# Optimization experiments

Measured on AMD Instinct MI355X. Metric: run time of the kernel, lower is better.

## Reference

```python
import jax, jax.numpy as jnp
import numpy as np

B, T, D = 8, 2048, 1024
E = 8               # num_experts
H = D // 8          # bottleneck dim = round(n_embed / reduction_rate) = 128


def setup_inputs() -> dict:
    key = jax.random.key(0)
    ks = jax.random.split(key, 7)
    s = 0.02
    return {
        "x":  jax.random.normal(ks[0], (B, T, D), dtype=jnp.float32),
        "Wr": jax.random.normal(ks[1], (D, E), dtype=jnp.float32) * s,
        "br": jnp.zeros((E,), dtype=jnp.float32),
        "Wd": jax.random.normal(ks[2], (E, D, H), dtype=jnp.float32) * s,
        "bd": jax.random.normal(ks[3], (E, H), dtype=jnp.float32) * s,
        "Wu": jax.random.normal(ks[4], (E, H, D), dtype=jnp.float32) * s,
        "bu": jax.random.normal(ks[5], (E, D), dtype=jnp.float32) * s,
    }


def reference(x, Wr, br, Wd, bd, Wu, bu):
    # Router: softmax over experts  -> [B, T, E]
    probs = jax.nn.softmax(x @ Wr + br, axis=-1)
    # All experts densely: down -> GELU (exact, matching torch.nn.GELU) -> up
    down = jnp.einsum('btd,edh->bteh', x, Wd) + bd            # [B, T, E, H]
    up = jnp.einsum('bteh,ehd->bted', jax.nn.gelu(down, approximate=False), Wu) + bu  # [B, T, E, D]
    # Router-weighted sum over experts -> [B, T, D]
    out = jnp.einsum('bte,bted->btd', probs, up)
    return out
```

## Files before the change

### kernel.cpp

```cpp
#include <hip/hip_runtime.h>

#define DEV __device__ __forceinline__

typedef short bf16x8 __attribute__((ext_vector_type(8)));
typedef float f32x4  __attribute__((ext_vector_type(4)));
typedef unsigned short u16;
typedef unsigned int u32;

constexpr int MTOK = 16384;
constexpr int DDIM = 1024;
constexpr int HDIM = 128;

constexpr int BM = 256, BN = 128, BK = 64;
constexpr int NKT = DDIM / BK;
constexpr int TA = BM * BK * 2;
constexpr int TB = BN * BK * 2;
constexpr int TT = TA + TB;

DEV u16 f2bf(float f) {
  u32 u = __builtin_bit_cast(u32, f);
  return (u16)((u + 0x7FFFu + ((u >> 16) & 1u)) >> 16);
}

DEV void async16(const void* g, void* l) {
  __builtin_amdgcn_global_load_lds(
      (const __attribute__((address_space(1))) void*)g,
      (__attribute__((address_space(3))) void*)l, 16, 0, 0);
}

__global__ __launch_bounds__(256) void prep_all_kernel(
    const float* __restrict__ x, const float* __restrict__ Wr,
    const float* __restrict__ br, const float* __restrict__ Wd,
    const float* __restrict__ Wu,
    u16* __restrict__ xh, u16* __restrict__ bdh, u16* __restrict__ wuh,
    float* __restrict__ probs)
{
  __shared__ float tl[32][33];
  const int bid = blockIdx.x;

  if (bid < 4096) {
    const int wave = threadIdx.x >> 6, lane = threadIdx.x & 63;
    const int t = bid * 4 + wave;
    const float* xr = x + (size_t)t * DDIM;

    float racc[8];
#pragma unroll
    for (int e = 0; e < 8; ++e) racc[e] = 0.f;

#pragma unroll
    for (int i = 0; i < 4; ++i) {
      const int d0 = i * 256 + lane * 4;
      float4 v = *(const float4*)(xr + d0);
      float vv[4] = {v.x, v.y, v.z, v.w};
      u16 hb[4];
#pragma unroll
      for (int j = 0; j < 4; ++j) {
        hb[j] = f2bf(vv[j]);
        const float4* w4 = (const float4*)(Wr + (size_t)(d0 + j) * 8);
        float4 w0 = w4[0], w1 = w4[1];
        racc[0] += vv[j] * w0.x; racc[1] += vv[j] * w0.y;
        racc[2] += vv[j] * w0.z; racc[3] += vv[j] * w0.w;
        racc[4] += vv[j] * w1.x; racc[5] += vv[j] * w1.y;
        racc[6] += vv[j] * w1.z; racc[7] += vv[j] * w1.w;
      }
      *(ushort4*)(xh + (size_t)t * DDIM + d0) = make_ushort4(hb[0], hb[1], hb[2], hb[3]);
    }

#pragma unroll
    for (int off = 32; off; off >>= 1)
#pragma unroll
      for (int e = 0; e < 8; ++e) racc[e] += __shfl_xor(racc[e], off, 64);

    float lg[8], mx = -1e30f;
#pragma unroll
    for (int e = 0; e < 8; ++e) { lg[e] = racc[e] + br[e]; mx = fmaxf(mx, lg[e]); }
    float ex[8], s = 0.f;
#pragma unroll
    for (int e = 0; e < 8; ++e) { ex[e] = expf(lg[e] - mx); s += ex[e]; }
    if (lane < 8) probs[(size_t)t * 8 + lane] = ex[lane] / s;
    return;
  }

  const float* src; u16* dst; int C; size_t dbase; int c0, r0;
  if (bid < 5120) {
    const int l = bid - 4096, e = l >> 7;
    src = Wd + (size_t)e * DDIM * HDIM; C = HDIM;
    dst = bdh; dbase = (size_t)e * HDIM * 1024;
    c0 = (l & 3) * 32; r0 = ((l >> 2) & 31) * 32;
  } else {
    const int l = bid - 5120, e = l >> 7;
    src = Wu + (size_t)e * HDIM * DDIM; C = DDIM;
    dst = wuh; dbase = (size_t)e * HDIM;
    c0 = (l & 31) * 32; r0 = ((l >> 5) & 3) * 32;
  }
  const int tx = threadIdx.x & 31, ty = threadIdx.x >> 5;
#pragma unroll
  for (int i = 0; i < 4; ++i)
    tl[ty + i * 8][tx] = src[(size_t)(r0 + ty + i * 8) * C + c0 + tx];
  __syncthreads();
#pragma unroll
  for (int i = 0; i < 4; ++i) {
    float v = tl[tx][ty + i * 8];
    dst[dbase + (size_t)(c0 + ty + i * 8) * 1024 + r0 + tx] = f2bf(v);
  }
}

template <int EPI>
__global__ __launch_bounds__(512, 2) void gemm_bf16_kernel(
    const u16* __restrict__ A, const u16* __restrict__ B,
    const float* __restrict__ bias, const float* __restrict__ probs,
    u16* __restrict__ ogp, float* __restrict__ of)
{
  __shared__ __align__(128) u16 lds[3 * TT / 2];
  const int tid = threadIdx.x, lane = tid & 63, wave = tid >> 6;
  const int wm = wave >> 1, wn = wave & 1;
  const int fr = lane & 15, fq = lane >> 4;

  const int swz = (blockIdx.x & 7) * 64 + (blockIdx.x >> 3);
  const int n0 = (swz >> 6) * BN;
  const int m0 = (swz & 63) * BM;

  auto stage = [&](int t) {
    u16* buf = lds + (size_t)(t % 3) * (TT / 2);
    const int kt = t * BK;
#pragma unroll
    for (int r = 0; r < 4; ++r) {
      const int off = r * 8192 + tid * 16;
      const int row = off >> 7, c = (off >> 4) & 7;
      const int sc = c ^ (row & 7);
      async16(A + (size_t)(m0 + row) * DDIM + kt + sc * 8, (char*)buf + off);
    }
#pragma unroll
    for (int r = 0; r < 2; ++r) {
      const int off = r * 8192 + tid * 16;
      const int row = off >> 7, c = (off >> 4) & 7;
      const int sc = c ^ (row & 7);
      async16(B + (size_t)(n0 + row) * DDIM + kt + sc * 8, (char*)buf + TA + off);
    }
  };

  f32x4 acc[4][4] = {};

  stage(0);
  stage(1);
  asm volatile("s_waitcnt vmcnt(6)" ::: "memory");
  __builtin_amdgcn_s_barrier();
  __builtin_amdgcn_sched_barrier(0);

  for (int t = 0; t < NKT; ++t) {
    if (t + 2 < NKT) stage(t + 2);

    const u16* At = lds + (size_t)(t % 3) * (TT / 2);
    const u16* Bt = At + TA / 2;
    bf16x8 a[2][4], b[2][4];
#pragma unroll
    for (int k2 = 0; k2 < 2; ++k2) {
      const int koff = k2 * 32 + fq * 8;
#pragma unroll
      for (int mi = 0; mi < 4; ++mi) {
        const int row = wm * 64 + mi * 16 + fr;
        int byt = (row << 7) + (koff << 1); byt ^= (row & 7) << 4;
        a[k2][mi] = *(const bf16x8*)((const char*)At + byt);
      }
#pragma unroll
      for (int ni = 0; ni < 4; ++ni) {
        const int row = wn * 64 + ni * 16 + fr;
        int byt = (row << 7) + (koff << 1); byt ^= (row & 7) << 4;
        b[k2][ni] = *(const bf16x8*)((const char*)Bt + byt);
      }
    }
    __builtin_amdgcn_s_setprio(1);
#pragma unroll
    for (int k2 = 0; k2 < 2; ++k2)
#pragma unroll
      for (int mi = 0; mi < 4; ++mi)
#pragma unroll
        for (int ni = 0; ni < 4; ++ni)
          acc[mi][ni] = __builtin_amdgcn_mfma_f32_16x16x32_bf16(
              a[k2][mi], b[k2][ni], acc[mi][ni], 0, 0, 0);
    __builtin_amdgcn_s_setprio(0);
    __builtin_amdgcn_sched_barrier(0);
    if (t < NKT - 2) asm volatile("s_waitcnt vmcnt(6)" ::: "memory");
    else             asm volatile("s_waitcnt vmcnt(0)" ::: "memory");
    __builtin_amdgcn_s_barrier();
    __builtin_amdgcn_sched_barrier(0);
  }

  if (EPI == 0) {
#pragma unroll
    for (int mi = 0; mi < 4; ++mi)
#pragma unroll
      for (int ni = 0; ni < 4; ++ni) {
        const int col = n0 + wn * 64 + ni * 16 + fr;
        const float bv = bias[col];
        const int e = col >> 7;
#pragma unroll
        for (int j = 0; j < 4; ++j) {
          const int row = m0 + wm * 64 + mi * 16 + fq * 4 + j;
          float v = acc[mi][ni][j] + bv;
          float g = 0.5f * v * (1.0f + erff(v * 0.70710678118654752f));
          ogp[(size_t)row * DDIM + col] = f2bf(probs[(size_t)row * 8 + e] * g);
        }
      }
  } else {
    float buv[4][8];
#pragma unroll
    for (int ni = 0; ni < 4; ++ni) {
      const int col = n0 + wn * 64 + ni * 16 + fr;
#pragma unroll
      for (int e = 0; e < 8; ++e) buv[ni][e] = bias[e * 1024 + col];
    }
#pragma unroll
    for (int mi = 0; mi < 4; ++mi)
#pragma unroll
      for (int j = 0; j < 4; ++j) {
        const int row = m0 + wm * 64 + mi * 16 + fq * 4 + j;
        const float4* pp = (const float4*)(probs + (size_t)row * 8);
        float4 p0 = pp[0], p1 = pp[1];
        float pr[8] = {p0.x, p0.y, p0.z, p0.w, p1.x, p1.y, p1.z, p1.w};
#pragma unroll
        for (int ni = 0; ni < 4; ++ni) {
          float v = acc[mi][ni][j];
#pragma unroll
          for (int e = 0; e < 8; ++e) v += pr[e] * buv[ni][e];
          of[(size_t)row * DDIM + n0 + wn * 64 + ni * 16 + fr] = v;
        }
      }
  }
}

extern "C" void kernel_launch(void* const* d_in, const int* in_sizes, int n_in,
                              void* d_out, int out_size, void* d_ws, size_t ws_size,
                              hipStream_t stream)
{
  const float* x  = (const float*)d_in[0];
  const float* Wr = (const float*)d_in[1];
  const float* br = (const float*)d_in[2];
  const float* Wd = (const float*)d_in[3];
  const float* bd = (const float*)d_in[4];
  const float* Wu = (const float*)d_in[5];
  const float* bu = (const float*)d_in[6];
  float* out = (float*)d_out;

  char* ws = (char*)d_ws;
  size_t off = 0;
  auto alloc = [&](size_t bytes) -> void* {
    void* p = ws + off;
    off += (bytes + 255) & ~(size_t)255;
    return p;
  };
  u16* xh  = (u16*)alloc((size_t)MTOK * DDIM * 2);
  u16* gph = (u16*)alloc((size_t)MTOK * 1024 * 2);
  u16* bdh = (u16*)alloc((size_t)1024 * 1024 * 2);
  u16* wuh = (u16*)alloc((size_t)1024 * 1024 * 2);
  float* probs = (float*)alloc((size_t)MTOK * 8 * 4);
  (void)ws_size; (void)in_sizes; (void)n_in; (void)out_size;

  prep_all_kernel<<<6144, 256, 0, stream>>>(x, Wr, br, Wd, Wu, xh, bdh, wuh, probs);

  gemm_bf16_kernel<0><<<512, 512, 0, stream>>>(xh, bdh, bd, probs, gph, nullptr);
  gemm_bf16_kernel<1><<<512, 512, 0, stream>>>(gph, wuh, bu, probs, nullptr, out);
}
```

Before: 287.9 us.

## Use 256x256 GEMM tiles with split-phase pipelining and an MFMA bf16 router

```diff
diff --git a/kernel.cpp b/kernel.cpp
--- a/kernel.cpp
+++ b/kernel.cpp
@@ -9,13 +9,8 @@
 
 constexpr int MTOK = 16384;
 constexpr int DDIM = 1024;
-constexpr int HDIM = 128;
-
-constexpr int BM = 256, BN = 128, BK = 64;
+constexpr int BK = 64;
 constexpr int NKT = DDIM / BK;
-constexpr int TA = BM * BK * 2;
-constexpr int TB = BN * BK * 2;
-constexpr int TT = TA + TB;
 
 DEV u16 f2bf(float f) {
   u32 u = __builtin_bit_cast(u32, f);
@@ -28,69 +23,46 @@
       (__attribute__((address_space(3))) void*)l, 16, 0, 0);
 }
 
-__global__ __launch_bounds__(256) void prep_all_kernel(
+#define LGKM0() asm volatile("s_waitcnt lgkmcnt(0)" ::: "memory")
+#define VMC(n)  asm volatile("s_waitcnt vmcnt(" #n ")" ::: "memory")
+#define SBAR()  __builtin_amdgcn_s_barrier()
+#define SCH0()  __builtin_amdgcn_sched_barrier(0)
+
+__global__ __launch_bounds__(256) void cast_kernel(
     const float* __restrict__ x, const float* __restrict__ Wr,
-    const float* __restrict__ br, const float* __restrict__ Wd,
-    const float* __restrict__ Wu,
-    u16* __restrict__ xh, u16* __restrict__ bdh, u16* __restrict__ wuh,
-    float* __restrict__ probs)
+    const float* __restrict__ Wd, const float* __restrict__ Wu,
+    u16* __restrict__ xh, u16* __restrict__ wrt,
+    u16* __restrict__ bdh, u16* __restrict__ wuh)
 {
+  const int bid = blockIdx.x;
+  if (bid < 1024) {
+    const int base = bid * 256 + threadIdx.x;
+#pragma unroll
+    for (int k = 0; k < 16; ++k) {
+      const size_t i = (size_t)base + (size_t)k * 262144;
+      float4 v = ((const float4*)x)[i];
+      ((ushort4*)xh)[i] = make_ushort4(f2bf(v.x), f2bf(v.y), f2bf(v.z), f2bf(v.w));
+    }
+    return;
+  }
+  if (bid >= 3072) {
+    for (int i = threadIdx.x; i < 16384; i += 256) {
+      const int e = i >> 10, d = i & 1023;
+      wrt[i] = (e < 8) ? f2bf(Wr[d * 8 + e]) : (u16)0;
+    }
+    return;
+  }
   __shared__ float tl[32][33];
-  const int bid = blockIdx.x;
-
-  if (bid < 4096) {
-    const int wave = threadIdx.x >> 6, lane = threadIdx.x & 63;
-    const int t = bid * 4 + wave;
-    const float* xr = x + (size_t)t * DDIM;
-
-    float racc[8];
-#pragma unroll
-    for (int e = 0; e < 8; ++e) racc[e] = 0.f;
-
-#pragma unroll
-    for (int i = 0; i < 4; ++i) {
-      const int d0 = i * 256 + lane * 4;
-      float4 v = *(const float4*)(xr + d0);
-      float vv[4] = {v.x, v.y, v.z, v.w};
-      u16 hb[4];
-#pragma unroll
-      for (int j = 0; j < 4; ++j) {
-        hb[j] = f2bf(vv[j]);
-        const float4* w4 = (const float4*)(Wr + (size_t)(d0 + j) * 8);
-        float4 w0 = w4[0], w1 = w4[1];
-        racc[0] += vv[j] * w0.x; racc[1] += vv[j] * w0.y;
-        racc[2] += vv[j] * w0.z; racc[3] += vv[j] * w0.w;
-        racc[4] += vv[j] * w1.x; racc[5] += vv[j] * w1.y;
-        racc[6] += vv[j] * w1.z; racc[7] += vv[j] * w1.w;
-      }
-      *(ushort4*)(xh + (size_t)t * DDIM + d0) = make_ushort4(hb[0], hb[1], hb[2], hb[3]);
-    }
-
-#pragma unroll
-    for (int off = 32; off; off >>= 1)
-#pragma unroll
-      for (int e = 0; e < 8; ++e) racc[e] += __shfl_xor(racc[e], off, 64);
-
-    float lg[8], mx = -1e30f;
-#pragma unroll
-    for (int e = 0; e < 8; ++e) { lg[e] = racc[e] + br[e]; mx = fmaxf(mx, lg[e]); }
-    float ex[8], s = 0.f;
-#pragma unroll
-    for (int e = 0; e < 8; ++e) { ex[e] = expf(lg[e] - mx); s += ex[e]; }
-    if (lane < 8) probs[(size_t)t * 8 + lane] = ex[lane] / s;
-    return;
-  }
-
   const float* src; u16* dst; int C; size_t dbase; int c0, r0;
-  if (bid < 5120) {
-    const int l = bid - 4096, e = l >> 7;
-    src = Wd + (size_t)e * DDIM * HDIM; C = HDIM;
-    dst = bdh; dbase = (size_t)e * HDIM * 1024;
+  if (bid < 2048) {
+    const int l = bid - 1024, e = l >> 7;
+    src = Wd + (size_t)e * DDIM * 128; C = 128;
+    dst = bdh; dbase = (size_t)e * 128 * 1024;
     c0 = (l & 3) * 32; r0 = ((l >> 2) & 31) * 32;
   } else {
-    const int l = bid - 5120, e = l >> 7;
-    src = Wu + (size_t)e * HDIM * DDIM; C = DDIM;
-    dst = wuh; dbase = (size_t)e * HDIM;
+    const int l = bid - 2048, e = l >> 7;
+    src = Wu + (size_t)e * 128 * DDIM; C = DDIM;
+    dst = wuh; dbase = (size_t)e * 128;
     c0 = (l & 31) * 32; r0 = ((l >> 5) & 3) * 32;
   }
   const int tx = threadIdx.x & 31, ty = threadIdx.x >> 5;
@@ -99,104 +71,184 @@
     tl[ty + i * 8][tx] = src[(size_t)(r0 + ty + i * 8) * C + c0 + tx];
   __syncthreads();
 #pragma unroll
-  for (int i = 0; i < 4; ++i) {
-    float v = tl[tx][ty + i * 8];
-    dst[dbase + (size_t)(c0 + ty + i * 8) * 1024 + r0 + tx] = f2bf(v);
-  }
-}
+  for (int i = 0; i < 4; ++i)
+    dst[dbase + (size_t)(c0 + ty + i * 8) * 1024 + r0 + tx] = f2bf(tl[tx][ty + i * 8]);
+}
+
+__global__ __launch_bounds__(256) void router_kernel(
+    const u16* __restrict__ xh, const u16* __restrict__ wrt,
+    const float* __restrict__ br, float* __restrict__ probs)
+{
+  __shared__ float red[4][64][16];
+  const int wave = threadIdx.x >> 6, lane = threadIdx.x & 63;
+  const int fr = lane & 15, fq = lane >> 4;
+  const int t0 = blockIdx.x * 64;
+  const int k0 = wave * 256;
+
+  f32x4 acc[4] = {};
+#pragma unroll
+  for (int ks = 0; ks < 8; ++ks) {
+    const int kc = k0 + ks * 32 + fq * 8;
+    bf16x8 b = *(const bf16x8*)&wrt[fr * 1024 + kc];
+#pragma unroll
+    for (int mi = 0; mi < 4; ++mi) {
+      bf16x8 a = *(const bf16x8*)&xh[(size_t)(t0 + mi * 16 + fr) * 1024 + kc];
+      acc[mi] = __builtin_amdgcn_mfma_f32_16x16x32_bf16(a, b, acc[mi], 0, 0, 0);
+    }
+  }
+#pragma unroll
+  for (int mi = 0; mi < 4; ++mi)
+#pragma unroll
+    for (int j = 0; j < 4; ++j)
+      red[wave][mi * 16 + fq * 4 + j][fr] = acc[mi][j];
+  __syncthreads();
+  const int row = threadIdx.x;
+  if (row < 64) {
+    float lg[8], mx = -1e30f;
+#pragma unroll
+    for (int e = 0; e < 8; ++e) {
+      float v = red[0][row][e] + red[1][row][e] + red[2][row][e] + red[3][row][e] + br[e];
+      lg[e] = v; mx = fmaxf(mx, v);
+    }
+    float s = 0.f;
+#pragma unroll
+    for (int e = 0; e < 8; ++e) { lg[e] = expf(lg[e] - mx); s += lg[e]; }
+    const float inv = 1.f / s;
+#pragma unroll
+    for (int e = 0; e < 8; ++e) probs[(size_t)(t0 + row) * 8 + e] = lg[e] * inv;
+  }
+}
+
+#define MFMA(a, b, c) __builtin_amdgcn_mfma_f32_16x16x32_bf16(a, b, c, 0, 0, 0)
 
 template <int EPI>
-__global__ __launch_bounds__(512, 2) void gemm_bf16_kernel(
-    const u16* __restrict__ A, const u16* __restrict__ B,
+__global__ __launch_bounds__(512, 2) void gemm8_kernel(
+    const u16* __restrict__ A, const u16* __restrict__ Bm,
     const float* __restrict__ bias, const float* __restrict__ probs,
     u16* __restrict__ ogp, float* __restrict__ of)
 {
-  __shared__ __align__(128) u16 lds[3 * TT / 2];
+  __shared__ __align__(128) char lds[131072];
   const int tid = threadIdx.x, lane = tid & 63, wave = tid >> 6;
-  const int wm = wave >> 1, wn = wave & 1;
+  const int wm = wave >> 2, wn = wave & 3;
   const int fr = lane & 15, fq = lane >> 4;
 
-  const int swz = (blockIdx.x & 7) * 64 + (blockIdx.x >> 3);
-  const int n0 = (swz >> 6) * BN;
-  const int m0 = (swz & 63) * BM;
-
-  auto stage = [&](int t) {
-    u16* buf = lds + (size_t)(t % 3) * (TT / 2);
+  const int wg = (blockIdx.x & 7) * 32 + (blockIdx.x >> 3);
+  const int n0 = (wg >> 6) * 256;
+  const int m0 = (wg & 63) * 256;
+
+  auto stage = [&](int t, int r) {
+    if (t >= NKT) return;
+    char* dst = lds + (t & 1) * 65536 + r * 16384;
+    const u16* src = (r < 2) ? A : Bm;
+    const int rbase = ((r < 2) ? m0 : n0) + (r & 1) * 128;
     const int kt = t * BK;
 #pragma unroll
-    for (int r = 0; r < 4; ++r) {
-      const int off = r * 8192 + tid * 16;
-      const int row = off >> 7, c = (off >> 4) & 7;
-      const int sc = c ^ (row & 7);
-      async16(A + (size_t)(m0 + row) * DDIM + kt + sc * 8, (char*)buf + off);
-    }
-#pragma unroll
-    for (int r = 0; r < 2; ++r) {
-      const int off = r * 8192 + tid * 16;
-      const int row = off >> 7, c = (off >> 4) & 7;
-      const int sc = c ^ (row & 7);
-      async16(B + (size_t)(n0 + row) * DDIM + kt + sc * 8, (char*)buf + TA + off);
+    for (int i = 0; i < 2; ++i) {
+      const int off = i * 8192 + tid * 16;
+      const int row = off >> 7;
+      const int sc = ((off >> 4) & 7) ^ (row & 7);
+      async16(src + (size_t)(rbase + row) * DDIM + kt + sc * 8, dst + off);
     }
   };
-
-  f32x4 acc[4][4] = {};
-
-  stage(0);
-  stage(1);
-  asm volatile("s_waitcnt vmcnt(6)" ::: "memory");
-  __builtin_amdgcn_s_barrier();
-  __builtin_amdgcn_sched_barrier(0);
-
+  auto ldsA = [&](int t, int mi, int k2) {
+    const int ar = wm * 128 + mi * 16 + fr;
+    const int off = (t & 1) * 65536 + (ar >> 7) * 16384 + (ar & 127) * 128
+                  + ((((k2 << 2) + fq) ^ (ar & 7)) << 4);
+    return *(const bf16x8*)(lds + off);
+  };
+  auto ldsB = [&](int t, int ni, int k2) {
+    const int brr = wn * 64 + ni * 16 + fr;
+    const int off = (t & 1) * 65536 + 32768 + (brr >> 7) * 16384 + (brr & 127) * 128
+                  + ((((k2 << 2) + fq) ^ (brr & 7)) << 4);
+    return *(const bf16x8*)(lds + off);
+  };
+
+  f32x4 acc[8][4] = {};
+
+  stage(0, 0); stage(0, 1); stage(0, 2); stage(0, 3);
+  stage(1, 2); stage(1, 3);
+  VMC(4); SBAR(); SCH0();
+
+#pragma unroll 2
   for (int t = 0; t < NKT; ++t) {
-    if (t + 2 < NKT) stage(t + 2);
-
-    const u16* At = lds + (size_t)(t % 3) * (TT / 2);
-    const u16* Bt = At + TA / 2;
-    bf16x8 a[2][4], b[2][4];
+    bf16x8 af[2][4], blo[2][2], bhi[2][2];
 #pragma unroll
     for (int k2 = 0; k2 < 2; ++k2) {
-      const int koff = k2 * 32 + fq * 8;
-#pragma unroll
-      for (int mi = 0; mi < 4; ++mi) {
-        const int row = wm * 64 + mi * 16 + fr;
-        int byt = (row << 7) + (koff << 1); byt ^= (row & 7) << 4;
-        a[k2][mi] = *(const bf16x8*)((const char*)At + byt);
-      }
-#pragma unroll
-      for (int ni = 0; ni < 4; ++ni) {
-        const int row = wn * 64 + ni * 16 + fr;
-        int byt = (row << 7) + (koff << 1); byt ^= (row & 7) << 4;
-        b[k2][ni] = *(const bf16x8*)((const char*)Bt + byt);
-      }
-    }
+#pragma unroll
+      for (int mi = 0; mi < 4; ++mi) af[k2][mi] = ldsA(t, mi, k2);
+#pragma unroll
+      for (int ni = 0; ni < 2; ++ni) blo[k2][ni] = ldsB(t, ni, k2);
+    }
+    stage(t + 1, 0);
+    SBAR(); LGKM0(); SCH0();
     __builtin_amdgcn_s_setprio(1);
 #pragma unroll
     for (int k2 = 0; k2 < 2; ++k2)
 #pragma unroll
       for (int mi = 0; mi < 4; ++mi)
 #pragma unroll
-        for (int ni = 0; ni < 4; ++ni)
-          acc[mi][ni] = __builtin_amdgcn_mfma_f32_16x16x32_bf16(
-              a[k2][mi], b[k2][ni], acc[mi][ni], 0, 0, 0);
+        for (int ni = 0; ni < 2; ++ni)
+          acc[mi][ni] = MFMA(af[k2][mi], blo[k2][ni], acc[mi][ni]);
     __builtin_amdgcn_s_setprio(0);
-    __builtin_amdgcn_sched_barrier(0);
-    if (t < NKT - 2) asm volatile("s_waitcnt vmcnt(6)" ::: "memory");
-    else             asm volatile("s_waitcnt vmcnt(0)" ::: "memory");
-    __builtin_amdgcn_s_barrier();
-    __builtin_amdgcn_sched_barrier(0);
+    SBAR(); SCH0();
+#pragma unroll
+    for (int k2 = 0; k2 < 2; ++k2)
+#pragma unroll
+      for (int ni = 0; ni < 2; ++ni) bhi[k2][ni] = ldsB(t, 2 + ni, k2);
+    stage(t + 1, 1);
+    SBAR(); LGKM0(); SCH0();
+    __builtin_amdgcn_s_setprio(1);
+#pragma unroll
+    for (int k2 = 0; k2 < 2; ++k2)
+#pragma unroll
+      for (int mi = 0; mi < 4; ++mi)
+#pragma unroll
+        for (int ni = 0; ni < 2; ++ni)
+          acc[mi][2 + ni] = MFMA(af[k2][mi], bhi[k2][ni], acc[mi][2 + ni]);
+    __builtin_amdgcn_s_setprio(0);
+    SBAR(); SCH0();
+#pragma unroll
+    for (int k2 = 0; k2 < 2; ++k2)
+#pragma unroll
+      for (int mi = 0; mi < 4; ++mi) af[k2][mi] = ldsA(t, 4 + mi, k2);
+    stage(t + 2, 2);
+    SBAR(); LGKM0(); SCH0();
+    __builtin_amdgcn_s_setprio(1);
+#pragma unroll
+    for (int k2 = 0; k2 < 2; ++k2)
+#pragma unroll
+      for (int mi = 0; mi < 4; ++mi)
+#pragma unroll
+        for (int ni = 0; ni < 2; ++ni)
+          acc[4 + mi][2 + ni] = MFMA(af[k2][mi], bhi[k2][ni], acc[4 + mi][2 + ni]);
+    __builtin_amdgcn_s_setprio(0);
+    SBAR(); SCH0();
+    stage(t + 2, 3);
+    if (t < NKT - 2) { VMC(4); } else { VMC(0); }
+    SBAR(); SCH0();
+    __builtin_amdgcn_s_setprio(1);
+#pragma unroll
+    for (int k2 = 0; k2 < 2; ++k2)
+#pragma unroll
+      for (int mi = 0; mi < 4; ++mi)
+#pragma unroll
+        for (int ni = 0; ni < 2; ++ni)
+          acc[4 + mi][ni] = MFMA(af[k2][mi], blo[k2][ni], acc[4 + mi][ni]);
+    __builtin_amdgcn_s_setprio(0);
+    SBAR(); SCH0();
   }
 
   if (EPI == 0) {
-#pragma unroll
-    for (int mi = 0; mi < 4; ++mi)
+    const int e = (n0 + wn * 64) >> 7;
+#pragma unroll
+    for (int mi = 0; mi < 8; ++mi)
 #pragma unroll
       for (int ni = 0; ni < 4; ++ni) {
         const int col = n0 + wn * 64 + ni * 16 + fr;
         const float bv = bias[col];
-        const int e = col >> 7;
 #pragma unroll
         for (int j = 0; j < 4; ++j) {
-          const int row = m0 + wm * 64 + mi * 16 + fq * 4 + j;
+          const int row = m0 + wm * 128 + mi * 16 + fq * 4 + j;
           float v = acc[mi][ni][j] + bv;
           float g = 0.5f * v * (1.0f + erff(v * 0.70710678118654752f));
           ogp[(size_t)row * DDIM + col] = f2bf(probs[(size_t)row * 8 + e] * g);
@@ -211,10 +263,10 @@
       for (int e = 0; e < 8; ++e) buv[ni][e] = bias[e * 1024 + col];
     }
 #pragma unroll
-    for (int mi = 0; mi < 4; ++mi)
+    for (int mi = 0; mi < 8; ++mi)
 #pragma unroll
       for (int j = 0; j < 4; ++j) {
-        const int row = m0 + wm * 64 + mi * 16 + fq * 4 + j;
+        const int row = m0 + wm * 128 + mi * 16 + fq * 4 + j;
         const float4* pp = (const float4*)(probs + (size_t)row * 8);
         float4 p0 = pp[0], p1 = pp[1];
         float pr[8] = {p0.x, p0.y, p0.z, p0.w, p1.x, p1.y, p1.z, p1.w};
@@ -253,11 +305,12 @@
   u16* gph = (u16*)alloc((size_t)MTOK * 1024 * 2);
   u16* bdh = (u16*)alloc((size_t)1024 * 1024 * 2);
   u16* wuh = (u16*)alloc((size_t)1024 * 1024 * 2);
+  u16* wrt = (u16*)alloc((size_t)16 * 1024 * 2);
   float* probs = (float*)alloc((size_t)MTOK * 8 * 4);
   (void)ws_size; (void)in_sizes; (void)n_in; (void)out_size;
 
-  prep_all_kernel<<<6144, 256, 0, stream>>>(x, Wr, br, Wd, Wu, xh, bdh, wuh, probs);
-
-  gemm_bf16_kernel<0><<<512, 512, 0, stream>>>(xh, bdh, bd, probs, gph, nullptr);
-  gemm_bf16_kernel<1><<<512, 512, 0, stream>>>(gph, wuh, bu, probs, nullptr, out);
-}
+  cast_kernel<<<3073, 256, 0, stream>>>(x, Wr, Wd, Wu, xh, wrt, bdh, wuh);
+  router_kernel<<<MTOK / 64, 256, 0, stream>>>(xh, wrt, br, probs);
+  gemm8_kernel<0><<<256, 512, 0, stream>>>(xh, bdh, bd, probs, gph, nullptr);
+  gemm8_kernel<1><<<256, 512, 0, stream>>>(gph, wuh, bu, probs, nullptr, out);
+}
```

After: 242.0 us. 1.19x faster.
